# Performance work log

Hardware: AMD Instinct MI355X
Metric: run time of the kernel (lower is better)

The kernel has to match this reference:

```python
import jax, jax.numpy as jnp
import numpy as np
from functools import partial

B, C_IN, IMG, P = 64, 3, 224, 16
D, DEPTH, H, MLP = 768, 12, 12, 3072
N = (IMG // P) ** 2 + 1  # 197 tokens (cls + patches)
HD = D // H
SCALE = HD ** -0.5
EPS = 1e-5
NCLS = 1000


def setup_inputs() -> dict:
    key = jax.random.key(0)
    ks = jax.random.split(key, 24)
    s = 0.02
    inp = {
        "x": jax.random.normal(ks[0], (B, C_IN, IMG, IMG), jnp.float32),
        "conv_w": jax.random.normal(ks[1], (D, C_IN, P, P), jnp.float32) * s,
        "conv_b": jnp.zeros((D,), jnp.float32),
        "cls_token": jax.random.normal(ks[2], (1, 1, D), jnp.float32) * 0.2,
        "pos_embed": jax.random.normal(ks[3], (1, N, D), jnp.float32) * 0.2,
        "qkv_w": jax.random.normal(ks[4], (DEPTH, 3 * D, D), jnp.float32) * s,
        "qkv_b": jax.random.normal(ks[5], (DEPTH, 3 * D), jnp.float32) * 1e-6,
        "proj_w": jax.random.normal(ks[6], (DEPTH, D, D), jnp.float32) * s,
        "proj_b": jax.random.normal(ks[7], (DEPTH, D), jnp.float32) * 1e-6,
        "n1_s": jnp.ones((DEPTH, D), jnp.float32),
        "n1_b": jnp.zeros((DEPTH, D), jnp.float32),
        "n2_s": jnp.ones((DEPTH, D), jnp.float32),
        "n2_b": jnp.zeros((DEPTH, D), jnp.float32),
        "fc1_w": jax.random.normal(ks[8], (DEPTH, MLP, D), jnp.float32) * s,
        "fc1_b": jax.random.normal(ks[9], (DEPTH, MLP), jnp.float32) * 1e-6,
        "fc2_w": jax.random.normal(ks[10], (DEPTH, D, MLP), jnp.float32) * s,
        "fc2_b": jax.random.normal(ks[11], (DEPTH, D), jnp.float32) * 1e-6,
        "enc_n_s": jnp.ones((D,), jnp.float32),
        "enc_n_b": jnp.zeros((D,), jnp.float32),
        "head_w": jnp.zeros((NCLS, D), jnp.float32),
        "head_b": jnp.zeros((NCLS,), jnp.float32),
    }
    return inp


def _ln(x, scale, bias):
    m = jnp.mean(x, axis=-1, keepdims=True)
    v = jnp.mean(jnp.square(x - m), axis=-1, keepdims=True)
    return (x - m) * jax.lax.rsqrt(v + EPS) * scale + bias


def _vit_forward(x, conv_w, conv_b, cls_token, pos_embed, qkv_w, qkv_b,
                 proj_w, proj_b, n1_s, n1_b, n2_s, n2_b, fc1_w, fc1_b,
                 fc2_w, fc2_b, enc_n_s, enc_n_b, head_w, head_b):
    bs = x.shape[0]
    # Patch embed: conv stride=kernel=16 -> [B, D, 14, 14] -> [B, 196, D]
    patches = jax.lax.conv_general_dilated(
        x, conv_w, window_strides=(P, P), padding="VALID",
        dimension_numbers=("NCHW", "OIHW", "NCHW")) + conv_b[None, :, None, None]
    patches = patches.reshape(bs, D, -1).transpose(0, 2, 1)  # [B, 196, D]
    h = jnp.concatenate([jnp.broadcast_to(cls_token, (bs, 1, D)), patches], axis=1)
    h = h + pos_embed  # [B, N, D]

    def block(h, p):
        qw, qb, pw, pb, s1, b1, s2, b2, f1w, f1b, f2w, f2b = p
        y = _ln(h, s1, b1)
        qkv = (y @ qw.T + qb).reshape(bs, N, 3, H, HD).transpose(2, 0, 3, 1, 4)
        q, k, v = qkv[0], qkv[1], qkv[2]  # each [B, H, N, HD]
        dot = jnp.einsum("bhid,bhjd->bhij", q, k) * SCALE
        attn = jax.nn.softmax(dot, axis=-1)
        o = jnp.einsum("bhij,bhjd->bhid", attn, v)
        o = o.transpose(0, 2, 1, 3).reshape(bs, N, D)
        h = h + (o @ pw.T + pb)
        y = _ln(h, s2, b2)
        y = jax.nn.gelu(y @ f1w.T + f1b, approximate=False) @ f2w.T + f2b
        return h + y, None

    params = (qkv_w, qkv_b, proj_w, proj_b, n1_s, n1_b, n2_s, n2_b,
              fc1_w, fc1_b, fc2_w, fc2_b)
    h, _ = jax.lax.scan(block, h, params)
    h = _ln(h, enc_n_s, enc_n_b)
    return h[:, 0] @ head_w.T + head_b  # [B, NCLS]


def reference(x, conv_w, conv_b, cls_token, pos_embed, qkv_w, qkv_b,
              proj_w, proj_b, n1_s, n1_b, n2_s, n2_b, fc1_w, fc1_b,
              fc2_w, fc2_b, enc_n_s, enc_n_b, head_w, head_b):
    return _vit_forward(x, conv_w, conv_b, cls_token, pos_embed, qkv_w, qkv_b,
                        proj_w, proj_b, n1_s, n1_b, n2_s, n2_b, fc1_w, fc1_b,
                        fc2_w, fc2_b, enc_n_s, enc_n_b, head_w, head_b)
```

## Files before the change

### kernel.cpp

```cpp
#include <hip/hip_runtime.h>
#include <hip/hip_bf16.h>

typedef __hip_bfloat16 bf16;
typedef __attribute__((ext_vector_type(8))) short bf16x8;
typedef __attribute__((ext_vector_type(4))) float f32x4;

#define B_SZ 64
#define D_MODEL 768
#define NTOK 197
#define MTOK (B_SZ * NTOK)
#define NHEAD 12
#define HDIM 64
#define MLP_DIM 3072
#define NCLS 1000

__device__ __forceinline__ void g2l16(const bf16* g, bf16* l) {
    __builtin_amdgcn_global_load_lds(
        (const __attribute__((address_space(1))) void*)g,
        (__attribute__((address_space(3))) void*)l, 16, 0, 0);
}

__global__ __launch_bounds__(256) void cvt_kernel(const float* __restrict__ in,
                                                  bf16* __restrict__ out, int n) {
    int i = ((int)blockIdx.x * 256 + (int)threadIdx.x) * 4;
    if (i >= n) return;
    float4 v = *(const float4*)(in + i);
    __align__(8) bf16 t[4] = {__float2bfloat16(v.x), __float2bfloat16(v.y),
                              __float2bfloat16(v.z), __float2bfloat16(v.w)};
    *(uint2*)(out + i) = *(uint2*)t;
}

#define R_QKV 1769472
#define R_PRJ 589824
#define R_FC  2359296
#define R_TOT 7077888
__global__ __launch_bounds__(256) void cvt_layer_kernel(
    const float* __restrict__ qw, const float* __restrict__ pw,
    const float* __restrict__ f1, const float* __restrict__ f2,
    bf16* __restrict__ out) {
    size_t i = ((size_t)blockIdx.x * 256 + threadIdx.x) * 4;
    const float* src;
    if (i < R_QKV)                src = qw + i;
    else if (i < R_QKV + R_PRJ)   src = pw + (i - R_QKV);
    else if (i < R_QKV + R_PRJ + R_FC) src = f1 + (i - R_QKV - R_PRJ);
    else                          src = f2 + (i - R_QKV - R_PRJ - R_FC);
    float4 v = *(const float4*)src;
    __align__(8) bf16 t[4] = {__float2bfloat16(v.x), __float2bfloat16(v.y),
                              __float2bfloat16(v.z), __float2bfloat16(v.w)};
    *(uint2*)(out + i) = *(uint2*)t;
}

__global__ __launch_bounds__(256) void im2row_kernel(const float* __restrict__ x,
                                                     bf16* __restrict__ out) {
    size_t idx = (size_t)blockIdx.x * 256 + threadIdx.x;
    int c = (int)(idx % 768);
    int r = (int)(idx / 768);
    int b = r / 196, pp = r % 196;
    int ph = pp / 14, pw = pp % 14;
    int ch = c >> 8, rem = c & 255;
    int i = rem >> 4, j = rem & 15;
    float v = x[(((size_t)b * 3 + ch) * 224 + ph * 16 + i) * 224 + pw * 16 + j];
    out[idx] = __float2bfloat16(v);
}

__global__ __launch_bounds__(256) void assemble_kernel(
    const float* __restrict__ pe, const float* __restrict__ cls,
    const float* __restrict__ pos, float* __restrict__ h) {
    size_t idx = (size_t)blockIdx.x * 256 + threadIdx.x;
    int d = (int)(idx % 768);
    size_t t_ = idx / 768;
    int t = (int)(t_ % 197);
    size_t b = t_ / 197;
    float v = (t == 0) ? cls[d] : pe[((size_t)b * 196 + (t - 1)) * 768 + d];
    h[idx] = v + pos[(size_t)t * 768 + d];
}

__global__ __launch_bounds__(256) void ln_kernel(
    const float* __restrict__ in, int row_stride,
    const float* __restrict__ sc, const float* __restrict__ bi,
    bf16* __restrict__ out) {
    const int row = blockIdx.x;
    const float* xr = in + (size_t)row * row_stride;
    const int tid = threadIdx.x;
    float v0 = xr[tid], v1 = xr[tid + 256], v2 = xr[tid + 512];
    float s = v0 + v1 + v2;
    float q = v0 * v0 + v1 * v1 + v2 * v2;
#pragma unroll
    for (int off = 32; off > 0; off >>= 1) {
        s += __shfl_down(s, off);
        q += __shfl_down(q, off);
    }
    __shared__ float sw[4], qw_[4];
    __shared__ float stat[2];
    int wv = tid >> 6;
    if ((tid & 63) == 0) { sw[wv] = s; qw_[wv] = q; }
    __syncthreads();
    if (tid == 0) {
        float S = sw[0] + sw[1] + sw[2] + sw[3];
        float Q = qw_[0] + qw_[1] + qw_[2] + qw_[3];
        float mean = S * (1.f / 768.f);
        float var = Q * (1.f / 768.f) - mean * mean;
        stat[0] = mean;
        stat[1] = rsqrtf(var + 1e-5f);
    }
    __syncthreads();
    float mean = stat[0], rstd = stat[1];
    size_t o0 = (size_t)row * 768;
    out[o0 + tid]       = __float2bfloat16((v0 - mean) * rstd * sc[tid]       + bi[tid]);
    out[o0 + tid + 256] = __float2bfloat16((v1 - mean) * rstd * sc[tid + 256] + bi[tid + 256]);
    out[o0 + tid + 512] = __float2bfloat16((v2 - mean) * rstd * sc[tid + 512] + bi[tid + 512]);
}

template <bool OUT_F32, bool RESID, bool GELU>
__global__ __launch_bounds__(256) void gemm_kernel(
    const bf16* __restrict__ A, const bf16* __restrict__ W,
    const float* __restrict__ bias, void* __restrict__ Cout,
    int M, int Nt, int K) {
    __shared__ __align__(16) bf16 As[128 * 64];
    __shared__ __align__(16) bf16 Bs[128 * 64];
    const int tid = threadIdx.x;
    const int lane = tid & 63;
    const int wave = tid >> 6;
    const int wm = wave >> 1, wn = wave & 1;
    const int m0 = blockIdx.y * 128, n0 = blockIdx.x * 128;
    const int m16 = lane & 15, kg = lane >> 4;

    f32x4 acc[4][4] = {};

    const int lr = lane >> 3;
    const int lc = ((lane & 7) ^ lr) * 8;
    const bf16* aptr[4];
    const bf16* bptr[4];
    bf16* alds[4];
    bf16* blds[4];
#pragma unroll
    for (int c = 0; c < 4; ++c) {
        int rsub = wave * 32 + c * 8;
        int ra = m0 + rsub + lr; ra = ra < M ? ra : M - 1;
        int rb = n0 + rsub + lr; rb = rb < Nt ? rb : Nt - 1;
        aptr[c] = A + (size_t)ra * K + lc;
        bptr[c] = W + (size_t)rb * K + lc;
        alds[c] = &As[rsub * 64];
        blds[c] = &Bs[rsub * 64];
    }

    for (int k0 = 0; k0 < K; k0 += 64) {
        __syncthreads();
#pragma unroll
        for (int c = 0; c < 4; ++c) g2l16(aptr[c] + k0, alds[c]);
#pragma unroll
        for (int c = 0; c < 4; ++c) g2l16(bptr[c] + k0, blds[c]);
        __syncthreads();
#pragma unroll
        for (int ks = 0; ks < 2; ++ks) {
            bf16x8 af[4], bfv[4];
            const int ch = ((ks << 2) + kg) ^ (m16 & 7);
#pragma unroll
            for (int t = 0; t < 4; ++t)
                af[t] = *(const bf16x8*)&As[(wm * 64 + t * 16 + m16) * 64 + (ch << 3)];
#pragma unroll
            for (int t = 0; t < 4; ++t)
                bfv[t] = *(const bf16x8*)&Bs[(wn * 64 + t * 16 + m16) * 64 + (ch << 3)];
#pragma unroll
            for (int i = 0; i < 4; ++i)
#pragma unroll
                for (int j = 0; j < 4; ++j)
                    acc[i][j] = __builtin_amdgcn_mfma_f32_16x16x32_bf16(
                        af[i], bfv[j], acc[i][j], 0, 0, 0);
        }
    }
    const int quad = lane >> 4;
#pragma unroll
    for (int i = 0; i < 4; ++i) {
        const int rbase = m0 + wm * 64 + i * 16 + quad * 4;
#pragma unroll
        for (int j = 0; j < 4; ++j) {
            const int col = n0 + wn * 64 + j * 16 + m16;
            if (col >= Nt) continue;
            const float bv = bias[col];
#pragma unroll
            for (int r = 0; r < 4; ++r) {
                const int row = rbase + r;
                if (row >= M) continue;
                float v = acc[i][j][r] + bv;
                if (GELU) v = 0.5f * v * (1.f + erff(v * 0.7071067811865476f));
                if (OUT_F32) {
                    float* op = (float*)Cout + (size_t)row * Nt + col;
                    if (RESID) *op += v; else *op = v;
                } else {
                    ((bf16*)Cout)[(size_t)row * Nt + col] = __float2bfloat16(v);
                }
            }
        }
    }
}

__global__ __launch_bounds__(256) void attn_kernel(const bf16* __restrict__ qkv,
                                                   bf16* __restrict__ o) {
    __shared__ __align__(16) bf16 Ks[208 * 72];
    __shared__ __align__(16) bf16 Vt[64 * 232];
    __shared__ __align__(16) bf16 Qs[32 * 72];
    __shared__ float Ss[32 * 209];
    __shared__ __align__(16) bf16 Ps[32 * 232];

    const int tid = threadIdx.x, lane = tid & 63, wave = tid >> 6;
    const int b = blockIdx.x / NHEAD, hh = blockIdx.x % NHEAD;
    const size_t base = (size_t)b * NTOK * 2304 + hh * 64;
    const int m16 = lane & 15, kg = lane >> 4, quad = lane >> 4;

    {
        const int jr = tid >> 3, ds = tid & 7;
        for (int j0 = 0; j0 < 224; j0 += 32) {
            int j = j0 + jr;
            if (j < 197) {
                int4 kv = *(const int4*)(qkv + base + 768 + (size_t)j * 2304 + ds * 8);
                *(int4*)&Ks[j * 72 + ds * 8] = kv;
                __align__(16) bf16 tmp[8];
                *(int4*)tmp = *(const int4*)(qkv + base + 1536 + (size_t)j * 2304 + ds * 8);
#pragma unroll
                for (int u = 0; u < 8; ++u) Vt[(ds * 8 + u) * 232 + j] = tmp[u];
            } else {
                if (j < 208) {
                    int4 z = make_int4(0, 0, 0, 0);
                    *(int4*)&Ks[j * 72 + ds * 8] = z;
                }
                bf16 zb = __float2bfloat16(0.f);
#pragma unroll
                for (int u = 0; u < 8; ++u) Vt[(ds * 8 + u) * 232 + j] = zb;
            }
        }
    }
    __syncthreads();

    for (int qt = 0; qt < 7; ++qt) {
        {
            const int r = tid >> 3, ds = tid & 7;
            int qi = qt * 32 + r;
            int4 v = make_int4(0, 0, 0, 0);
            if (qi < 197) v = *(const int4*)(qkv + base + (size_t)qi * 2304 + ds * 8);
            *(int4*)&Qs[r * 72 + ds * 8] = v;
        }
        __syncthreads();
        bf16x8 qf[2][2];
#pragma unroll
        for (int mt = 0; mt < 2; ++mt)
#pragma unroll
            for (int ks = 0; ks < 2; ++ks)
                qf[mt][ks] = *(const bf16x8*)&Qs[(mt * 16 + m16) * 72 + ks * 32 + kg * 8];
        for (int nt = wave; nt < 13; nt += 4) {
            f32x4 s0 = {0.f, 0.f, 0.f, 0.f}, s1 = {0.f, 0.f, 0.f, 0.f};
#pragma unroll
            for (int ks = 0; ks < 2; ++ks) {
                bf16x8 kf = *(const bf16x8*)&Ks[(nt * 16 + m16) * 72 + ks * 32 + kg * 8];
                s0 = __builtin_amdgcn_mfma_f32_16x16x32_bf16(qf[0][ks], kf, s0, 0, 0, 0);
                s1 = __builtin_amdgcn_mfma_f32_16x16x32_bf16(qf[1][ks], kf, s1, 0, 0, 0);
            }
            const int col = nt * 16 + m16;
#pragma unroll
            for (int r = 0; r < 4; ++r) {
                Ss[(quad * 4 + r) * 209 + col]        = s0[r] * 0.125f;
                Ss[(16 + quad * 4 + r) * 209 + col]   = s1[r] * 0.125f;
            }
        }
        __syncthreads();
        {
            const int r = tid >> 3, c0 = tid & 7;
            const float* srow = &Ss[r * 209];
            float mx = -3.0e38f;
            for (int c = c0; c < 197; c += 8) mx = fmaxf(mx, srow[c]);
#pragma unroll
            for (int off = 4; off > 0; off >>= 1) mx = fmaxf(mx, __shfl_xor(mx, off, 8));
            float l = 0.f;
            for (int c = c0; c < 197; c += 8) l += __expf(srow[c] - mx);
#pragma unroll
            for (int off = 4; off > 0; off >>= 1) l += __shfl_xor(l, off, 8);
            const float inv = 1.f / l;
            bf16* prow = &Ps[r * 232];
            for (int c = c0; c < 224; c += 8)
                prow[c] = __float2bfloat16(c < 197 ? __expf(srow[c] - mx) * inv : 0.f);
        }
        __syncthreads();
        f32x4 o0 = {0.f, 0.f, 0.f, 0.f}, o1 = {0.f, 0.f, 0.f, 0.f};
#pragma unroll
        for (int ks = 0; ks < 7; ++ks) {
            bf16x8 vf = *(const bf16x8*)&Vt[(wave * 16 + m16) * 232 + ks * 32 + kg * 8];
            bf16x8 p0 = *(const bf16x8*)&Ps[m16 * 232 + ks * 32 + kg * 8];
            bf16x8 p1 = *(const bf16x8*)&Ps[(16 + m16) * 232 + ks * 32 + kg * 8];
            o0 = __builtin_amdgcn_mfma_f32_16x16x32_bf16(p0, vf, o0, 0, 0, 0);
            o1 = __builtin_amdgcn_mfma_f32_16x16x32_bf16(p1, vf, o1, 0, 0, 0);
        }
        const int dcol = hh * 64 + wave * 16 + m16;
#pragma unroll
        for (int r = 0; r < 4; ++r) {
            int q0i = qt * 32 + quad * 4 + r;
            if (q0i < 197) o[((size_t)b * NTOK + q0i) * 768 + dcol] = __float2bfloat16(o0[r]);
            int q1i = qt * 32 + 16 + quad * 4 + r;
            if (q1i < 197) o[((size_t)b * NTOK + q1i) * 768 + dcol] = __float2bfloat16(o1[r]);
        }
    }
}

extern "C" void kernel_launch(void* const* d_in, const int* in_sizes, int n_in,
                              void* d_out, int out_size, void* d_ws, size_t ws_size,
                              hipStream_t stream) {
    const float* x      = (const float*)d_in[0];
    const float* conv_w = (const float*)d_in[1];
    const float* conv_b = (const float*)d_in[2];
    const float* cls_t  = (const float*)d_in[3];
    const float* pos    = (const float*)d_in[4];
    const float* qkv_w  = (const float*)d_in[5];
    const float* qkv_b  = (const float*)d_in[6];
    const float* proj_w = (const float*)d_in[7];
    const float* proj_b = (const float*)d_in[8];
    const float* n1_s   = (const float*)d_in[9];
    const float* n1_b   = (const float*)d_in[10];
    const float* n2_s   = (const float*)d_in[11];
    const float* n2_b   = (const float*)d_in[12];
    const float* fc1_w  = (const float*)d_in[13];
    const float* fc1_b  = (const float*)d_in[14];
    const float* fc2_w  = (const float*)d_in[15];
    const float* fc2_b  = (const float*)d_in[16];
    const float* enc_s  = (const float*)d_in[17];
    const float* enc_b  = (const float*)d_in[18];
    const float* head_w = (const float*)d_in[19];
    const float* head_b = (const float*)d_in[20];

    char* p = (char*)d_ws;
    auto take = [&](size_t bytes) -> char* {
        char* r = p;
        p += (bytes + 255) & ~(size_t)255;
        return r;
    };
    bf16* wb_layer = (bf16*)take((size_t)R_TOT * 2);
    bf16* wb_conv  = (bf16*)take((size_t)589824 * 2);
    bf16* wb_head  = (bf16*)take((size_t)NCLS * 768 * 2);
    float* h       = (float*)take((size_t)MTOK * 768 * 4);
    bf16* y        = (bf16*)take((size_t)MTOK * 768 * 2);
    char* qkv_raw  = take((size_t)MTOK * 2304 * 2);
    bf16* qkvb     = (bf16*)qkv_raw;
    float* pe_out  = (float*)qkv_raw;
    bf16* o        = (bf16*)take((size_t)MTOK * 768 * 2);
    char* mid_raw  = take((size_t)MTOK * 3072 * 2);
    bf16* mid      = (bf16*)mid_raw;
    bf16* peA      = (bf16*)mid_raw;
    bf16* yh       = (bf16*)take((size_t)128 * 768 * 2);

    cvt_kernel<<<576, 256, 0, stream>>>(conv_w, wb_conv, 589824);
    cvt_kernel<<<750, 256, 0, stream>>>(head_w, wb_head, NCLS * 768);
    im2row_kernel<<<37632, 256, 0, stream>>>(x, peA);
    gemm_kernel<true, false, false><<<dim3(6, 98), 256, 0, stream>>>(
        peA, wb_conv, conv_b, pe_out, 12544, 768, 768);
    assemble_kernel<<<37824, 256, 0, stream>>>(pe_out, cls_t, pos, h);

    for (int l = 0; l < 12; ++l) {
        cvt_layer_kernel<<<R_TOT / 4 / 256, 256, 0, stream>>>(
            qkv_w + (size_t)l * R_QKV, proj_w + (size_t)l * R_PRJ,
            fc1_w + (size_t)l * R_FC, fc2_w + (size_t)l * R_FC, wb_layer);
        ln_kernel<<<MTOK, 256, 0, stream>>>(h, 768, n1_s + l * 768, n1_b + l * 768, y);
        gemm_kernel<false, false, false><<<dim3(18, 99), 256, 0, stream>>>(
            y, wb_layer, qkv_b + l * 2304, qkvb, MTOK, 2304, 768);
        attn_kernel<<<768, 256, 0, stream>>>(qkvb, o);
        gemm_kernel<true, true, false><<<dim3(6, 99), 256, 0, stream>>>(
            o, wb_layer + R_QKV, proj_b + l * 768, h, MTOK, 768, 768);
        ln_kernel<<<MTOK, 256, 0, stream>>>(h, 768, n2_s + l * 768, n2_b + l * 768, y);
        gemm_kernel<false, false, true><<<dim3(24, 99), 256, 0, stream>>>(
            y, wb_layer + R_QKV + R_PRJ, fc1_b + l * 3072, mid, MTOK, 3072, 768);
        gemm_kernel<true, true, false><<<dim3(6, 99), 256, 0, stream>>>(
            mid, wb_layer + R_QKV + R_PRJ + R_FC, fc2_b + l * 768, h, MTOK, 768, 3072);
    }

    ln_kernel<<<64, 256, 0, stream>>>(h, NTOK * 768, enc_s, enc_b, yh);
    gemm_kernel<true, false, false><<<dim3(8, 1), 256, 0, stream>>>(
        yh, wb_head, head_b, (float*)d_out, 64, NCLS, 768);
}
```

Baseline: 6.733 ms.

## Pre-transpose V and keep attention softmax in registers with swizzled LDS

A new kernel transposes V into a per-head [64 x 224] buffer so the attention kernel can load it with direct global-to-LDS copies. K is loaded the same way. The attention kernel keeps the score tiles in registers and does the softmax max and sum reductions with lane shuffles plus a small cross-wave LDS exchange, which removes the fp32 score buffer. LDS tiles now use XOR swizzling in place of padding, to avoid bank conflicts. The cost is an extra kernel launch per layer and an extra global round trip for V, and vT is placed at an offset inside the mid buffer, which is only safe if that region is not live at the time.

```diff
diff --git a/kernel.cpp b/kernel.cpp
--- a/kernel.cpp
+++ b/kernel.cpp
@@ -195,97 +195,226 @@
     }
 }
 
+__global__ __launch_bounds__(256) void trv_kernel(const bf16* __restrict__ qkv,
+                                                  bf16* __restrict__ vT) {
+    __shared__ __align__(16) bf16 T[64 * 72];
+    const int tid = threadIdx.x;
+    const int bh = blockIdx.x >> 2;
+    const int j0 = (blockIdx.x & 3) * 64;
+    const int b = bh / NHEAD, hh = bh % NHEAD;
+    const size_t vbase = (size_t)b * NTOK * 2304 + 1536 + (size_t)hh * 64;
+    {
+        int j = tid >> 2;
+        int jj = j0 + j;
+        int cpair = (tid & 3) * 2;
+#pragma unroll
+        for (int cc = 0; cc < 2; ++cc) {
+            int c = cpair + cc;
+            int4 v = make_int4(0, 0, 0, 0);
+            if (jj < 197) v = *(const int4*)(qkv + vbase + (size_t)jj * 2304 + c * 8);
+            *(int4*)&T[j * 72 + c * 8] = v;
+        }
+    }
+    __syncthreads();
+    {
+        int d = tid >> 2;
+#pragma unroll
+        for (int cc = 0; cc < 2; ++cc) {
+            int lch = (tid & 3) + cc * 4;
+            __align__(16) bf16 tmp[8];
+#pragma unroll
+            for (int u = 0; u < 8; ++u) tmp[u] = T[(lch * 8 + u) * 72 + d];
+            *(int4*)(vT + ((size_t)bh * 64 + d) * 224 + j0 + lch * 8) = *(int4*)tmp;
+        }
+    }
+}
+
 __global__ __launch_bounds__(256) void attn_kernel(const bf16* __restrict__ qkv,
+                                                   const bf16* __restrict__ vT,
                                                    bf16* __restrict__ o) {
-    __shared__ __align__(16) bf16 Ks[208 * 72];
-    __shared__ __align__(16) bf16 Vt[64 * 232];
-    __shared__ __align__(16) bf16 Qs[32 * 72];
-    __shared__ float Ss[32 * 209];
-    __shared__ __align__(16) bf16 Ps[32 * 232];
+    __shared__ __align__(16) bf16 Ks[208 * 64];
+    __shared__ __align__(16) bf16 Vt[64 * 256];
+    __shared__ __align__(16) bf16 Qs[32 * 64];
+    __shared__ __align__(16) bf16 Ps[32 * 256];
+    __shared__ float pmax[4][32];
+    __shared__ float psum[4][32];
 
     const int tid = threadIdx.x, lane = tid & 63, wave = tid >> 6;
-    const int b = blockIdx.x / NHEAD, hh = blockIdx.x % NHEAD;
+    const int bh = blockIdx.x;
+    const int b = bh / NHEAD, hh = bh % NHEAD;
     const size_t base = (size_t)b * NTOK * 2304 + hh * 64;
     const int m16 = lane & 15, kg = lane >> 4, quad = lane >> 4;
 
     {
-        const int jr = tid >> 3, ds = tid & 7;
-        for (int j0 = 0; j0 < 224; j0 += 32) {
-            int j = j0 + jr;
-            if (j < 197) {
-                int4 kv = *(const int4*)(qkv + base + 768 + (size_t)j * 2304 + ds * 8);
-                *(int4*)&Ks[j * 72 + ds * 8] = kv;
-                __align__(16) bf16 tmp[8];
-                *(int4*)tmp = *(const int4*)(qkv + base + 1536 + (size_t)j * 2304 + ds * 8);
-#pragma unroll
-                for (int u = 0; u < 8; ++u) Vt[(ds * 8 + u) * 232 + j] = tmp[u];
-            } else {
-                if (j < 208) {
-                    int4 z = make_int4(0, 0, 0, 0);
-                    *(int4*)&Ks[j * 72 + ds * 8] = z;
-                }
-                bf16 zb = __float2bfloat16(0.f);
-#pragma unroll
-                for (int u = 0; u < 8; ++u) Vt[(ds * 8 + u) * 232 + j] = zb;
-            }
+        const int lr = lane >> 3, lc7 = lane & 7;
+        for (int g = wave; g < 25; g += 4) {
+            int row = g * 8 + lr;
+            if (row < 197)
+                g2l16(qkv + base + 768 + (size_t)row * 2304 + ((lc7 ^ lr) * 8),
+                      &Ks[g * 512]);
+        }
+        if (tid < 88) {
+            int row = 197 + tid / 8, ch = tid % 8;
+            *(int4*)&Ks[row * 64 + ch * 8] = make_int4(0, 0, 0, 0);
+        }
+        if (tid < 64) {
+            int row = tid >> 1, c = 26 + (tid & 1);
+            *(int4*)&Ps[row * 256 + ((c ^ (row & 7)) * 8)] = make_int4(0, 0, 0, 0);
+        }
+        const int vr = lane >> 5, vp = lane & 31;
+        for (int g = wave; g < 32; g += 4) {
+            int row = g * 2 + vr;
+            int c = vp ^ (row & 7);
+            int cc = c < 28 ? c : 27;
+            g2l16(vT + ((size_t)bh * 64 + row) * 224 + cc * 8, &Vt[g * 512]);
         }
     }
     __syncthreads();
 
     for (int qt = 0; qt < 7; ++qt) {
         {
-            const int r = tid >> 3, ds = tid & 7;
+            int r = tid >> 3, c = tid & 7;
             int qi = qt * 32 + r;
             int4 v = make_int4(0, 0, 0, 0);
-            if (qi < 197) v = *(const int4*)(qkv + base + (size_t)qi * 2304 + ds * 8);
-            *(int4*)&Qs[r * 72 + ds * 8] = v;
+            if (qi < 197) v = *(const int4*)(qkv + base + (size_t)qi * 2304 + c * 8);
+            *(int4*)&Qs[r * 64 + ((c ^ (r & 7)) * 8)] = v;
         }
         __syncthreads();
+
         bf16x8 qf[2][2];
 #pragma unroll
         for (int mt = 0; mt < 2; ++mt)
 #pragma unroll
             for (int ks = 0; ks < 2; ++ks)
-                qf[mt][ks] = *(const bf16x8*)&Qs[(mt * 16 + m16) * 72 + ks * 32 + kg * 8];
-        for (int nt = wave; nt < 13; nt += 4) {
-            f32x4 s0 = {0.f, 0.f, 0.f, 0.f}, s1 = {0.f, 0.f, 0.f, 0.f};
-#pragma unroll
-            for (int ks = 0; ks < 2; ++ks) {
-                bf16x8 kf = *(const bf16x8*)&Ks[(nt * 16 + m16) * 72 + ks * 32 + kg * 8];
-                s0 = __builtin_amdgcn_mfma_f32_16x16x32_bf16(qf[0][ks], kf, s0, 0, 0, 0);
-                s1 = __builtin_amdgcn_mfma_f32_16x16x32_bf16(qf[1][ks], kf, s1, 0, 0, 0);
+                qf[mt][ks] = *(const bf16x8*)
+                    &Qs[(mt * 16 + m16) * 64 + (((ks * 4 + kg) ^ (m16 & 7)) * 8)];
+
+        f32x4 sacc[2][4];
+#pragma unroll
+        for (int mt = 0; mt < 2; ++mt)
+#pragma unroll
+            for (int t = 0; t < 4; ++t) sacc[mt][t] = (f32x4){0.f, 0.f, 0.f, 0.f};
+#pragma unroll
+        for (int t = 0; t < 4; ++t) {
+            int nt = wave + 4 * t;
+            if (nt < 13) {
+#pragma unroll
+                for (int ks = 0; ks < 2; ++ks) {
+                    bf16x8 kf = *(const bf16x8*)
+                        &Ks[(nt * 16 + m16) * 64 + (((ks * 4 + kg) ^ (m16 & 7)) * 8)];
+                    sacc[0][t] = __builtin_amdgcn_mfma_f32_16x16x32_bf16(
+                        qf[0][ks], kf, sacc[0][t], 0, 0, 0);
+                    sacc[1][t] = __builtin_amdgcn_mfma_f32_16x16x32_bf16(
+                        qf[1][ks], kf, sacc[1][t], 0, 0, 0);
+                }
             }
-            const int col = nt * 16 + m16;
+        }
+        float pm[2][4];
+#pragma unroll
+        for (int mt = 0; mt < 2; ++mt)
+#pragma unroll
+            for (int r = 0; r < 4; ++r) pm[mt][r] = -3.0e38f;
+#pragma unroll
+        for (int t = 0; t < 4; ++t) {
+            int nt = wave + 4 * t;
+            bool v = (nt * 16 + m16) < 197;
+#pragma unroll
+            for (int mt = 0; mt < 2; ++mt)
+#pragma unroll
+                for (int r = 0; r < 4; ++r) {
+                    float x = sacc[mt][t][r] * 0.125f;
+                    sacc[mt][t][r] = x;
+                    if (v) pm[mt][r] = fmaxf(pm[mt][r], x);
+                }
+        }
+#pragma unroll
+        for (int off = 1; off < 16; off <<= 1)
+#pragma unroll
+            for (int mt = 0; mt < 2; ++mt)
+#pragma unroll
+                for (int r = 0; r < 4; ++r)
+                    pm[mt][r] = fmaxf(pm[mt][r], __shfl_xor(pm[mt][r], off));
+        if (m16 == 0) {
+#pragma unroll
+            for (int mt = 0; mt < 2; ++mt)
+#pragma unroll
+                for (int r = 0; r < 4; ++r)
+                    pmax[wave][mt * 16 + quad * 4 + r] = pm[mt][r];
+        }
+        __syncthreads();
+        float fm[2][4];
+#pragma unroll
+        for (int mt = 0; mt < 2; ++mt)
 #pragma unroll
             for (int r = 0; r < 4; ++r) {
-                Ss[(quad * 4 + r) * 209 + col]        = s0[r] * 0.125f;
-                Ss[(16 + quad * 4 + r) * 209 + col]   = s1[r] * 0.125f;
+                int row = mt * 16 + quad * 4 + r;
+                fm[mt][r] = fmaxf(fmaxf(pmax[0][row], pmax[1][row]),
+                                  fmaxf(pmax[2][row], pmax[3][row]));
             }
+        float ps[2][4] = {};
+#pragma unroll
+        for (int t = 0; t < 4; ++t) {
+            int nt = wave + 4 * t;
+            bool v = (nt * 16 + m16) < 197;
+#pragma unroll
+            for (int mt = 0; mt < 2; ++mt)
+#pragma unroll
+                for (int r = 0; r < 4; ++r) {
+                    float e = v ? __expf(sacc[mt][t][r] - fm[mt][r]) : 0.f;
+                    sacc[mt][t][r] = e;
+                    ps[mt][r] += e;
+                }
+        }
+#pragma unroll
+        for (int off = 1; off < 16; off <<= 1)
+#pragma unroll
+            for (int mt = 0; mt < 2; ++mt)
+#pragma unroll
+                for (int r = 0; r < 4; ++r)
+                    ps[mt][r] += __shfl_xor(ps[mt][r], off);
+        if (m16 == 0) {
+#pragma unroll
+            for (int mt = 0; mt < 2; ++mt)
+#pragma unroll
+                for (int r = 0; r < 4; ++r)
+                    psum[wave][mt * 16 + quad * 4 + r] = ps[mt][r];
         }
         __syncthreads();
-        {
-            const int r = tid >> 3, c0 = tid & 7;
-            const float* srow = &Ss[r * 209];
-            float mx = -3.0e38f;
-            for (int c = c0; c < 197; c += 8) mx = fmaxf(mx, srow[c]);
-#pragma unroll
-            for (int off = 4; off > 0; off >>= 1) mx = fmaxf(mx, __shfl_xor(mx, off, 8));
-            float l = 0.f;
-            for (int c = c0; c < 197; c += 8) l += __expf(srow[c] - mx);
-#pragma unroll
-            for (int off = 4; off > 0; off >>= 1) l += __shfl_xor(l, off, 8);
-            const float inv = 1.f / l;
-            bf16* prow = &Ps[r * 232];
-            for (int c = c0; c < 224; c += 8)
-                prow[c] = __float2bfloat16(c < 197 ? __expf(srow[c] - mx) * inv : 0.f);
+        float inv[2][4];
+#pragma unroll
+        for (int mt = 0; mt < 2; ++mt)
+#pragma unroll
+            for (int r = 0; r < 4; ++r) {
+                int row = mt * 16 + quad * 4 + r;
+                inv[mt][r] = 1.f / (psum[0][row] + psum[1][row] +
+                                    psum[2][row] + psum[3][row]);
+            }
+#pragma unroll
+        for (int t = 0; t < 4; ++t) {
+            int nt = wave + 4 * t;
+            int col = nt * 16 + m16;
+            if (col < 208) {
+#pragma unroll
+                for (int mt = 0; mt < 2; ++mt)
+#pragma unroll
+                    for (int r = 0; r < 4; ++r) {
+                        int row = mt * 16 + quad * 4 + r;
+                        Ps[row * 256 + (((col >> 3) ^ (row & 7)) * 8) + (col & 7)] =
+                            __float2bfloat16(sacc[mt][t][r] * inv[mt][r]);
+                    }
+            }
         }
         __syncthreads();
         f32x4 o0 = {0.f, 0.f, 0.f, 0.f}, o1 = {0.f, 0.f, 0.f, 0.f};
+        const int vrow = wave * 16 + m16;
 #pragma unroll
         for (int ks = 0; ks < 7; ++ks) {
-            bf16x8 vf = *(const bf16x8*)&Vt[(wave * 16 + m16) * 232 + ks * 32 + kg * 8];
-            bf16x8 p0 = *(const bf16x8*)&Ps[m16 * 232 + ks * 32 + kg * 8];
-            bf16x8 p1 = *(const bf16x8*)&Ps[(16 + m16) * 232 + ks * 32 + kg * 8];
+            bf16x8 vf = *(const bf16x8*)
+                &Vt[vrow * 256 + (((ks * 4 + kg) ^ (vrow & 7)) * 8)];
+            bf16x8 p0 = *(const bf16x8*)
+                &Ps[m16 * 256 + (((ks * 4 + kg) ^ (m16 & 7)) * 8)];
+            bf16x8 p1 = *(const bf16x8*)
+                &Ps[(16 + m16) * 256 + (((ks * 4 + kg) ^ (m16 & 7)) * 8)];
             o0 = __builtin_amdgcn_mfma_f32_16x16x32_bf16(p0, vf, o0, 0, 0, 0);
             o1 = __builtin_amdgcn_mfma_f32_16x16x32_bf16(p1, vf, o1, 0, 0, 0);
         }
@@ -343,6 +472,7 @@
     char* mid_raw  = take((size_t)MTOK * 3072 * 2);
     bf16* mid      = (bf16*)mid_raw;
     bf16* peA      = (bf16*)mid_raw;
+    bf16* vT       = (bf16*)(mid_raw + (size_t)40 * 1024 * 1024);
     bf16* yh       = (bf16*)take((size_t)128 * 768 * 2);
 
     cvt_kernel<<<576, 256, 0, stream>>>(conv_w, wb_conv, 589824);
@@ -359,7 +489,8 @@
         ln_kernel<<<MTOK, 256, 0, stream>>>(h, 768, n1_s + l * 768, n1_b + l * 768, y);
         gemm_kernel<false, false, false><<<dim3(18, 99), 256, 0, stream>>>(
             y, wb_layer, qkv_b + l * 2304, qkvb, MTOK, 2304, 768);
-        attn_kernel<<<768, 256, 0, stream>>>(qkvb, o);
+        trv_kernel<<<3072, 256, 0, stream>>>(qkvb, vT);
+        attn_kernel<<<768, 256, 0, stream>>>(qkvb, vT, o);
         gemm_kernel<true, true, false><<<dim3(6, 99), 256, 0, stream>>>(
             o, wb_layer + R_QKV, proj_b + l * 768, h, MTOK, 768, 768);
         ln_kernel<<<MTOK, 256, 0, stream>>>(h, 768, n2_s + l * 768, n2_b + l * 768, y);
```

New measurement: 6.058 ms. 1.11x faster.
